# Optimization experiments

Hardware: AMD Instinct MI355X
Metric: run time of the kernel (lower is better)

The kernel has to match this reference:

```python
import jax, jax.numpy as jnp
import numpy as np

# arch = "12;cache:15,gaussian:4,identity:2,sin:1" -> segments and activations
# d_hidden = [15, 4, 2, 1], sum = 22; activations = [cache(identity), gaussian, identity, sin]
N_LAYERS = 12
D_HIDDEN = 22


def _gaussian(x):
    return jnp.exp(-x ** 2) * 2.0 - 1.0


def _act(h):
    # split into segments [15,4,2,1], apply per-segment activation, concat
    return jnp.concatenate([
        h[..., 0:15],            # cache == identity
        _gaussian(h[..., 15:19]),# gaussian
        h[..., 19:21],           # identity
        jnp.sin(h[..., 21:22]),  # sin
    ], axis=-1)


def setup_inputs() -> dict:
    key = jax.random.key(0)
    k1, k2, k3, k4 = jax.random.split(key, 4)
    N = 524288
    x = jax.random.normal(k1, (N, 4), dtype=jnp.float32)
    # lecun-style scaling (variance_scaling fan_in) approximated with scaled normal
    w_in = jax.random.normal(k2, (4, D_HIDDEN), dtype=jnp.float32) / jnp.sqrt(4.0)
    w_hidden = jax.random.normal(k3, (N_LAYERS - 1, D_HIDDEN, D_HIDDEN), dtype=jnp.float32) / jnp.sqrt(float(D_HIDDEN))
    w_out = jax.random.normal(k4, (D_HIDDEN, 3), dtype=jnp.float32) / jnp.sqrt(float(D_HIDDEN))
    return {"x": x, "w_in": w_in, "w_hidden": w_hidden, "w_out": w_out}


def reference(x, w_in, w_hidden, w_out):
    # Vectorized over pixels (batch dim N) instead of per-pixel vmap.
    features = [x]
    h = _act(jnp.einsum('ni,io->no', x, w_in))  # layer 0: [N,4]x[4,22]
    features.append(h)
    for i in range(N_LAYERS - 1):  # small fixed layer count, structurally distinct weights
        h = _act(jnp.einsum('nd,de->ne', h, w_hidden[i]))
        features.append(h)
    out = jnp.einsum('nd,do->no', h, w_out)  # [N,3] = (h,s,v)
    features.append(out)
    return (out, *features)
```

## Files before the change

### kernel.cpp

```cpp
#include <hip/hip_runtime.h>

#define NPIX 524288
#define DH 22
#define NHID 11
#define TPB 256
#define WTILE (64*DH)

typedef float f32x4 __attribute__((ext_vector_type(4)));
typedef float f32x2 __attribute__((ext_vector_type(2)));

__device__ __forceinline__ void activate(float* h) {
#pragma unroll
    for (int j = 15; j < 19; ++j) h[j] = __expf(-h[j]*h[j]) * 2.0f - 1.0f;
    h[21] = __sinf(h[21]);
}

__device__ __forceinline__ void hidden_layer(float* __restrict__ h,
                                             const float* __restrict__ W) {
    float hn[DH];
#pragma unroll
    for (int o = 0; o < DH; ++o) hn[o] = 0.0f;
#pragma unroll
    for (int i = 0; i < DH; ++i) {
        const float hi = h[i];
#pragma unroll
        for (int o = 0; o < DH; ++o)
            hn[o] = fmaf(hi, W[i*DH + o], hn[o]);
    }
    activate(hn);
#pragma unroll
    for (int o = 0; o < DH; ++o) h[o] = hn[o];
}

__device__ __forceinline__ void flush_h(float* __restrict__ gwave,
                                        const float* __restrict__ h,
                                        float* __restrict__ wlds, int lane) {
    f32x2* d = (f32x2*)(wlds + lane * DH);
#pragma unroll
    for (int k = 0; k < 11; ++k) { f32x2 v2 = { h[2*k], h[2*k+1] }; d[k] = v2; }
    const f32x4* s4 = (const f32x4*)wlds;
    f32x4* g4 = (f32x4*)gwave;
#pragma unroll
    for (int k = 0; k < 5; ++k) {
        const int s = lane + 64 * k;
        __builtin_nontemporal_store(s4[s], &g4[s]);
    }
    if (lane < 32) {
        const int s = 320 + lane;
        __builtin_nontemporal_store(s4[s], &g4[s]);
    }
}

__global__ __launch_bounds__(256) void cppn_main(const float* __restrict__ xin,
                                                 const float* __restrict__ Win,
                                                 const float* __restrict__ Whid,
                                                 const float* __restrict__ Wout,
                                                 float* __restrict__ out) {
    __shared__ float lds[4][WTILE];
    const int t    = threadIdx.x;
    const int w    = t >> 6;
    const int lane = t & 63;
    const int blk  = blockIdx.x;
    const int p    = blk * TPB + t;
    float* wlds = lds[w];

    const f32x4 xv = ((const f32x4*)xin)[p];
    __builtin_nontemporal_store(xv, &((f32x4*)(out + (size_t)3 * NPIX))[p]);

    float h[DH];
#pragma unroll
    for (int o = 0; o < DH; ++o) {
        float a =      xv.x * Win[0*DH + o];
        a = fmaf(xv.y, Win[1*DH + o], a);
        a = fmaf(xv.z, Win[2*DH + o], a);
        a = fmaf(xv.w, Win[3*DH + o], a);
        h[o] = a;
    }
    activate(h);

    float* hwave = out + (size_t)7 * NPIX + (size_t)blk * (TPB * DH) + w * WTILE;
    const size_t chunk = (size_t)NPIX * DH;

    flush_h(hwave, h, wlds, lane);
    for (int l = 0; l < NHID; ++l) {
        hidden_layer(h, Whid + (size_t)l * DH * DH);
        flush_h(hwave + (size_t)(l + 1) * chunk, h, wlds, lane);
    }

    float o0 = 0.0f, o1 = 0.0f, o2 = 0.0f;
#pragma unroll
    for (int d = 0; d < DH; ++d) {
        o0 = fmaf(h[d], Wout[d*3 + 0], o0);
        o1 = fmaf(h[d], Wout[d*3 + 1], o1);
        o2 = fmaf(h[d], Wout[d*3 + 2], o2);
    }
    wlds[lane*3 + 0] = o0; wlds[lane*3 + 1] = o1; wlds[lane*3 + 2] = o2;
    if (lane < 48) {
        const f32x4 v = ((const f32x4*)wlds)[lane];
        const size_t s = (size_t)blk * 192 + w * 48 + lane;
        __builtin_nontemporal_store(v, &((f32x4*)out)[s]);
        __builtin_nontemporal_store(v, &((f32x4*)(out + (size_t)271 * NPIX))[s]);
    }
}

extern "C" void kernel_launch(void* const* d_in, const int* in_sizes, int n_in,
                              void* d_out, int out_size, void* d_ws, size_t ws_size,
                              hipStream_t stream) {
    const float* x     = (const float*)d_in[0];
    const float* w_in  = (const float*)d_in[1];
    const float* w_hid = (const float*)d_in[2];
    const float* w_out = (const float*)d_in[3];
    float* o = (float*)d_out;

    cppn_main<<<NPIX / TPB, TPB, 0, stream>>>(x, w_in, w_hid, w_out, o);
}
```

Measured before the change: 118.4 us.

## Software-pipeline hidden-state flushes behind next layer's matmul with sched barriers

```diff
diff --git a/kernel.cpp b/kernel.cpp
--- a/kernel.cpp
+++ b/kernel.cpp
@@ -15,40 +15,10 @@
     h[21] = __sinf(h[21]);
 }
 
-__device__ __forceinline__ void hidden_layer(float* __restrict__ h,
-                                             const float* __restrict__ W) {
-    float hn[DH];
-#pragma unroll
-    for (int o = 0; o < DH; ++o) hn[o] = 0.0f;
-#pragma unroll
-    for (int i = 0; i < DH; ++i) {
-        const float hi = h[i];
-#pragma unroll
-        for (int o = 0; o < DH; ++o)
-            hn[o] = fmaf(hi, W[i*DH + o], hn[o]);
-    }
-    activate(hn);
-#pragma unroll
-    for (int o = 0; o < DH; ++o) h[o] = hn[o];
-}
-
-__device__ __forceinline__ void flush_h(float* __restrict__ gwave,
-                                        const float* __restrict__ h,
-                                        float* __restrict__ wlds, int lane) {
+__device__ __forceinline__ void write_tile(float* __restrict__ wlds, const float* h, int lane) {
     f32x2* d = (f32x2*)(wlds + lane * DH);
 #pragma unroll
-    for (int k = 0; k < 11; ++k) { f32x2 v2 = { h[2*k], h[2*k+1] }; d[k] = v2; }
-    const f32x4* s4 = (const f32x4*)wlds;
-    f32x4* g4 = (f32x4*)gwave;
-#pragma unroll
-    for (int k = 0; k < 5; ++k) {
-        const int s = lane + 64 * k;
-        __builtin_nontemporal_store(s4[s], &g4[s]);
-    }
-    if (lane < 32) {
-        const int s = 320 + lane;
-        __builtin_nontemporal_store(s4[s], &g4[s]);
-    }
+    for (int k = 0; k < 11; ++k) { f32x2 v = { h[2*k], h[2*k+1] }; d[k] = v; }
 }
 
 __global__ __launch_bounds__(256) void cppn_main(const float* __restrict__ xin,
@@ -77,15 +47,52 @@
         h[o] = a;
     }
     activate(h);
+    write_tile(wlds, h, lane);
 
     float* hwave = out + (size_t)7 * NPIX + (size_t)blk * (TPB * DH) + w * WTILE;
     const size_t chunk = (size_t)NPIX * DH;
+    const f32x2* s2 = (const f32x2*)wlds;
 
-    flush_h(hwave, h, wlds, lane);
+#pragma unroll 1
     for (int l = 0; l < NHID; ++l) {
-        hidden_layer(h, Whid + (size_t)l * DH * DH);
-        flush_h(hwave + (size_t)(l + 1) * chunk, h, wlds, lane);
+        f32x2 sd[11];
+#pragma unroll
+        for (int k = 0; k < 11; ++k) sd[k] = s2[lane + 64*k];
+
+        const float* W = Whid + (size_t)l * DH * DH;
+        float hn[DH];
+#pragma unroll
+        for (int o = 0; o < DH; ++o) hn[o] = 0.0f;
+#pragma unroll
+        for (int i = 0; i < DH; ++i) {
+            const float hi = h[i];
+#pragma unroll
+            for (int o = 0; o < DH; ++o)
+                hn[o] = fmaf(hi, W[i*DH + o], hn[o]);
+        }
+
+        f32x2* g2 = (f32x2*)(hwave + (size_t)l * chunk);
+#pragma unroll
+        for (int k = 0; k < 11; ++k)
+            __builtin_nontemporal_store(sd[k], &g2[lane + 64*k]);
+
+        activate(hn);
+#pragma unroll
+        for (int o = 0; o < DH; ++o) h[o] = hn[o];
+        write_tile(wlds, h, lane);
+
+        __builtin_amdgcn_sched_group_barrier(0x100, 11, 0);
+#pragma unroll
+        for (int k = 0; k < 11; ++k) {
+            __builtin_amdgcn_sched_group_barrier(0x40, 1, 0);
+            __builtin_amdgcn_sched_group_barrier(0x2, 44, 0);
+        }
+        __builtin_amdgcn_sched_group_barrier(0x200, 11, 0);
     }
+
+    f32x2 sd[11];
+#pragma unroll
+    for (int k = 0; k < 11; ++k) sd[k] = s2[lane + 64*k];
 
     float o0 = 0.0f, o1 = 0.0f, o2 = 0.0f;
 #pragma unroll
@@ -94,6 +101,13 @@
         o1 = fmaf(h[d], Wout[d*3 + 1], o1);
         o2 = fmaf(h[d], Wout[d*3 + 2], o2);
     }
+    {
+        f32x2* g2 = (f32x2*)(hwave + (size_t)NHID * chunk);
+#pragma unroll
+        for (int k = 0; k < 11; ++k)
+            __builtin_nontemporal_store(sd[k], &g2[lane + 64*k]);
+    }
+
     wlds[lane*3 + 0] = o0; wlds[lane*3 + 1] = o1; wlds[lane*3 + 2] = o2;
     if (lane < 48) {
         const f32x4 v = ((const f32x4*)wlds)[lane];
```

Result: slower. 144.9 us (+22.4%).
